# Performance work log

Hardware: AMD Instinct MI355X
Metric: run time of the kernel (lower is better)

The kernel has to match this reference:

```python
import jax, jax.numpy as jnp
from jax import lax
import numpy as np

B, T = 16, 64
NC, CS, HID, FEAT, ADIM = 32, 32, 128, 256, 6
CAT = NC * CS  # 1024


def _conv(x, w, b):
    # kernel 4, stride 2, padding 1 (NCHW / OIHW)
    y = lax.conv_general_dilated(x, w, window_strides=(2, 2), padding=[(1, 1), (1, 1)],
                                 dimension_numbers=('NCHW', 'OIHW', 'NCHW'))
    return y + b[None, :, None, None]


def _ln(x, g, b, eps=1e-5):
    # nn.LayerNorm([C,H,W]) normalizes over the last 3 dims with full affine
    m = jnp.mean(x, axis=(1, 2, 3), keepdims=True)
    v = jnp.var(x, axis=(1, 2, 3), keepdims=True)
    return (x - m) * lax.rsqrt(v + eps) * g[None] + b[None]


def setup_inputs() -> dict:
    key = jax.random.key(0)
    ks = jax.random.split(key, 12)
    w = lambda k, s: jax.random.normal(k, s, jnp.float32) * 0.02
    d = {
        'states': jax.random.normal(ks[0], (B, T, 3, 64, 64), jnp.float32),
        'actions': jax.random.normal(ks[1], (B, T, ADIM), jnp.float32),
        'conv1_w': w(ks[2], (32, 3, 4, 4)), 'conv1_b': jnp.zeros((32,), jnp.float32),
        'ln1_g': jnp.ones((32, 32, 32), jnp.float32), 'ln1_b': jnp.zeros((32, 32, 32), jnp.float32),
        'conv2_w': w(ks[3], (64, 32, 4, 4)), 'conv2_b': jnp.zeros((64,), jnp.float32),
        'ln2_g': jnp.ones((64, 16, 16), jnp.float32), 'ln2_b': jnp.zeros((64, 16, 16), jnp.float32),
        'conv3_w': w(ks[4], (128, 64, 4, 4)), 'conv3_b': jnp.zeros((128,), jnp.float32),
        'ln3_g': jnp.ones((128, 8, 8), jnp.float32), 'ln3_b': jnp.zeros((128, 8, 8), jnp.float32),
        'conv4_w': w(ks[5], (256, 128, 4, 4)), 'conv4_b': jnp.zeros((256,), jnp.float32),
        'ln4_g': jnp.ones((256, 4, 4), jnp.float32), 'ln4_b': jnp.zeros((256, 4, 4), jnp.float32),
        'fc_w': w(ks[6], (FEAT, 256 * 4 * 4)), 'fc_b': jnp.zeros((FEAT,), jnp.float32),
        'gru_wih': w(ks[7], (3 * HID, CAT + ADIM)), 'gru_whh': w(ks[8], (3 * HID, HID)),
        'gru_bih': jnp.zeros((3 * HID,), jnp.float32), 'gru_bhh': jnp.zeros((3 * HID,), jnp.float32),
        'prior_w': w(ks[9], (CAT, HID)), 'prior_b': jnp.zeros((CAT,), jnp.float32),
        'post_w': w(ks[10], (CAT, HID + FEAT)), 'post_b': jnp.zeros((CAT,), jnp.float32),
    }
    return d


def reference(states, actions, conv1_w, conv1_b, ln1_g, ln1_b, conv2_w, conv2_b, ln2_g, ln2_b,
              conv3_w, conv3_b, ln3_g, ln3_b, conv4_w, conv4_b, ln4_g, ln4_b, fc_w, fc_b,
              gru_wih, gru_whh, gru_bih, gru_bhh, prior_w, prior_b, post_w, post_b):
    bt = B * T
    # Encoder has no recurrent dependency -> batch all frames at once.
    x = states.reshape(bt, 3, 64, 64)
    x = jax.nn.silu(_ln(_conv(x, conv1_w, conv1_b), ln1_g, ln1_b))
    x = jax.nn.silu(_ln(_conv(x, conv2_w, conv2_b), ln2_g, ln2_b))
    x = jax.nn.silu(_ln(_conv(x, conv3_w, conv3_b), ln3_g, ln3_b))
    x = jax.nn.silu(_ln(_conv(x, conv4_w, conv4_b), ln4_g, ln4_b))
    feats = x.reshape(bt, -1) @ fc_w.T + fc_b              # [B*T, FEAT]
    feats = feats.reshape(B, T, FEAT).transpose(1, 0, 2)    # [T, B, FEAT]
    acts = actions.transpose(1, 0, 2)                       # [T, B, A]

    def step(carry, inp):
        h, z = carry
        a, f = inp
        xg = jnp.concatenate([z, a], axis=-1)
        gi = xg @ gru_wih.T + gru_bih
        gh = h @ gru_whh.T + gru_bhh
        ir, iz, inn = jnp.split(gi, 3, axis=-1)
        hr, hz, hn = jnp.split(gh, 3, axis=-1)
        r = jax.nn.sigmoid(ir + hr)
        u = jax.nn.sigmoid(iz + hz)
        n = jnp.tanh(inn + r * hn)
        h_new = (1.0 - u) * n + u * h                      # PyTorch GRUCell update
        prior = (h_new @ prior_w.T + prior_b).reshape(B, NC, CS)
        post = (jnp.concatenate([h_new, f], axis=-1) @ post_w.T + post_b).reshape(B, NC, CS)
        # eval-mode sampling: one-hot argmax (deterministic)
        z_new = jax.nn.one_hot(jnp.argmax(post, axis=-1), CS, dtype=h_new.dtype).reshape(B, CAT)
        return (h_new, z_new), (prior, post, h_new, z_new)

    init = (jnp.zeros((B, HID), states.dtype), jnp.zeros((B, CAT), states.dtype))
    _, (prior_l, post_l, h_seq, z_seq) = lax.scan(step, init, (acts, feats))
    return (prior_l.transpose(1, 0, 2, 3), post_l.transpose(1, 0, 2, 3),
            h_seq.transpose(1, 0, 2), z_seq.transpose(1, 0, 2))
```

## Files before the change

### kernel.cpp

```cpp
#include <hip/hip_runtime.h>
#include <math.h>


__device__ __forceinline__ float silu_f(float t){ return t / (1.f + __expf(-t)); }
__device__ __forceinline__ float sigm_f(float x){ return 1.f / (1.f + expf(-x)); }

__device__ __forceinline__ void block_stats_256(float s, float s2, int m,
                                                float& mean, float& rstd)
{
    __shared__ float red[8];
#pragma unroll
    for (int off = 32; off > 0; off >>= 1) {
        s  += __shfl_down(s, off);
        s2 += __shfl_down(s2, off);
    }
    int wv = threadIdx.x >> 6;
    if ((threadIdx.x & 63) == 0) { red[wv] = s; red[4 + wv] = s2; }
    __syncthreads();
    if (threadIdx.x == 0) {
        float S  = (red[0] + red[1]) + (red[2] + red[3]);
        float S2 = (red[4] + red[5]) + (red[6] + red[7]);
        float mu = S / m;
        float var = S2 / m - mu * mu;
        red[0] = mu;
        red[1] = rsqrtf(var + 1e-5f);
    }
    __syncthreads();
    mean = red[0]; rstd = red[1];
}

__global__ __launch_bounds__(256) void ln_fuse_k(float* __restrict__ x,
    const float* __restrict__ g, const float* __restrict__ b, int m)
{
    int n = blockIdx.x;
    float* p = x + (size_t)n * m;
    float s = 0.f, s2 = 0.f;
    for (int i = threadIdx.x * 4; i < m; i += 1024) {
        float4 v = *(const float4*)(p + i);
        s  += (v.x + v.y) + (v.z + v.w);
        s2 += (v.x*v.x + v.y*v.y) + (v.z*v.z + v.w*v.w);
    }
    float mean, rstd;
    block_stats_256(s, s2, m, mean, rstd);
    for (int i = threadIdx.x * 4; i < m; i += 1024) {
        float4 v  = *(float4*)(p + i);
        float4 gv = *(const float4*)(g + i);
        float4 bv = *(const float4*)(b + i);
        v.x = silu_f((v.x - mean) * rstd * gv.x + bv.x);
        v.y = silu_f((v.y - mean) * rstd * gv.y + bv.y);
        v.z = silu_f((v.z - mean) * rstd * gv.z + bv.z);
        v.w = silu_f((v.w - mean) * rstd * gv.w + bv.w);
        *(float4*)(p + i) = v;
    }
}

__global__ __launch_bounds__(256) void conv1_k(const float* __restrict__ in,
    const float* __restrict__ w, const float* __restrict__ bias, float* __restrict__ out)
{
    int n  = blockIdx.x;
    int yq = blockIdx.y;
    int tx = threadIdx.x & 31;
    int ty = threadIdx.x >> 5;
    int y  = yq * 8 + ty;
    const float* ip = in + (size_t)n * 12288;

    float okf[16]; int offs[16];
#pragma unroll
    for (int ky = 0; ky < 4; ky++) {
        int yy = 2 * y - 1 + ky;
        bool yok = ((unsigned)yy < 64u);
#pragma unroll
        for (int kx = 0; kx < 4; kx++) {
            int xx = 2 * tx - 1 + kx;
            bool ok = yok && ((unsigned)xx < 64u);
            okf[ky*4+kx]  = ok ? 1.f : 0.f;
            offs[ky*4+kx] = ok ? yy * 64 + xx : 0;
        }
    }
    float iv[48];
#pragma unroll
    for (int c = 0; c < 3; c++)
#pragma unroll
        for (int q = 0; q < 16; q++)
            iv[c*16+q] = ip[c*4096 + offs[q]] * okf[q];

    float* op = out + (size_t)n * 32768 + y * 32 + tx;
#pragma unroll 4
    for (int oc = 0; oc < 32; oc++) {
        float acc = bias[oc];
        const float* wp = w + oc * 48;
#pragma unroll
        for (int q = 0; q < 48; q++) acc += iv[q] * wp[q];
        op[oc * 1024] = acc;
    }
}

__global__ __launch_bounds__(256) void conv2_r(const float* __restrict__ in,
    const float* __restrict__ w, const float* __restrict__ bias, float* __restrict__ out)
{
    __shared__ __align__(16) float lds[8208];
    int n  = blockIdx.x;
    int tid = threadIdx.x;
    int wv  = tid >> 6;
    int g   = wv >> 1;
    int s   = ((wv & 1) << 6) | (tid & 63);
    int x   = s & 15, y0 = s >> 4;
    const float* ip = in + (size_t)n * 32768;

    int offs[2][16];
#pragma unroll
    for (int p = 0; p < 2; p++) {
        int y = y0 + 8 * p;
#pragma unroll
        for (int ky = 0; ky < 4; ky++) {
            int yi = 2 * y - 1 + ky;
#pragma unroll
            for (int kx = 0; kx < 4; kx++) {
                int xi = 2 * x - 1 + kx;
                bool ok = ((unsigned)yi < 32u) && ((unsigned)xi < 32u);
                int rot = ((xi >> 2) + (yi & 7)) & 7;
                int foff = yi * 32 + rot * 4 + (xi & 3);
                offs[p][ky*4+kx] = ok ? (4 + foff) * 4 : 0;
            }
        }
    }
    if (tid < 16) lds[(tid >> 2) * 1028 + (tid & 3)] = 0.f;

    float acc0[32], acc1[32];
#pragma unroll
    for (int i = 0; i < 32; i++) { float bv = bias[g*32 + i]; acc0[i] = bv; acc1[i] = bv; }

#pragma unroll 1
    for (int ch = 0; ch < 8; ch++) {
        __syncthreads();
        {
            const float4* gs = (const float4*)(ip + (ch << 12));
#pragma unroll
            for (int k = 0; k < 4; k++) {
                int gid = tid + (k << 8);
                int cc = gid >> 8, r = (gid >> 3) & 31, s4 = gid & 7;
                int rs = (s4 + (r & 7)) & 7;
                *(float4*)&lds[cc*1028 + 4 + r*32 + rs*4] = gs[gid];
            }
            int oc = tid >> 2, i4 = tid & 3;
            const float* wg = w + (size_t)oc * 512 + (ch << 6) + i4 * 4;
#pragma unroll
            for (int cc = 0; cc < 4; cc++)
                *(float4*)&lds[4112 + cc*1024 + oc*16 + i4*4] =
                    *(const float4*)(wg + cc * 16);
        }
        __syncthreads();
#pragma unroll 1
        for (int cc = 0; cc < 4; cc++) {
            const char* cb = (const char*)lds + cc * 4112;
            float iv0[16], iv1[16];
#pragma unroll
            for (int q = 0; q < 16; q++) {
                iv0[q] = *(const float*)(cb + offs[0][q]);
                iv1[q] = *(const float*)(cb + offs[1][q]);
            }
            const float* wb = &lds[4112 + cc*1024 + g*512];
#pragma unroll
            for (int o = 0; o < 32; o++) {
                float wt[16];
                *(float4*)&wt[0]  = *(const float4*)(wb + o*16);
                *(float4*)&wt[4]  = *(const float4*)(wb + o*16 + 4);
                *(float4*)&wt[8]  = *(const float4*)(wb + o*16 + 8);
                *(float4*)&wt[12] = *(const float4*)(wb + o*16 + 12);
#pragma unroll
                for (int q = 0; q < 16; q++) {
                    acc0[o] = fmaf(iv0[q], wt[q], acc0[o]);
                    acc1[o] = fmaf(iv1[q], wt[q], acc1[o]);
                }
            }
        }
    }
    float* op = out + (size_t)n * 16384;
#pragma unroll
    for (int o = 0; o < 32; o++) {
        op[(g*32 + o) * 256 + y0*16 + x]       = acc0[o];
        op[(g*32 + o) * 256 + (y0+8)*16 + x]   = acc1[o];
    }
}

__global__ __launch_bounds__(256) void conv3_r(const float* __restrict__ in,
    const float* __restrict__ w, const float* __restrict__ bias, float* __restrict__ out)
{
    __shared__ __align__(16) float lds[9232];
    int n   = blockIdx.x;
    int tid = threadIdx.x;
    int g   = tid >> 5;
    int slot= tid & 31;
    int x   = slot & 7, y0 = slot >> 3;

    int offs[2][16];
#pragma unroll
    for (int p = 0; p < 2; p++) {
        int y = y0 + 4 * p;
#pragma unroll
        for (int ky = 0; ky < 4; ky++) {
            int yi = 2 * y - 1 + ky;
#pragma unroll
            for (int kx = 0; kx < 4; kx++) {
                int xi = 2 * x - 1 + kx;
                bool ok = ((unsigned)yi < 16u) && ((unsigned)xi < 16u);
                int rot = ((xi >> 2) + (yi & 3)) & 3;
                int foff = yi * 16 + rot * 4 + (xi & 3);
                offs[p][ky*4+kx] = ok ? (4 + foff) * 4 : 0;
            }
        }
    }
    if (tid < 16) lds[(tid >> 2) * 260 + (tid & 3)] = 0.f;

    float acc0[16], acc1[16];
#pragma unroll
    for (int i = 0; i < 16; i++) { float bv = bias[g*16 + i]; acc0[i] = bv; acc1[i] = bv; }

    const float* ip = in + (size_t)n * 16384;
#pragma unroll 1
    for (int ch = 0; ch < 16; ch++) {
        __syncthreads();
        {
            const float4* gs = (const float4*)(ip + (ch << 10));
            int cc = tid >> 6, r = (tid >> 2) & 15, s4 = tid & 3;
            int rs = (s4 + (r & 3)) & 3;
            *(float4*)&lds[cc*260 + 4 + r*16 + rs*4] = gs[tid];
            int oc = tid >> 1, h = tid & 1;
            const float* wg = w + (size_t)oc * 1024 + (ch << 6) + h * 8;
#pragma unroll
            for (int c2 = 0; c2 < 4; c2++) {
                *(float4*)&lds[1040 + c2*2048 + oc*16 + h*8]     = *(const float4*)(wg + c2*16);
                *(float4*)&lds[1040 + c2*2048 + oc*16 + h*8 + 4] = *(const float4*)(wg + c2*16 + 4);
            }
        }
        __syncthreads();
#pragma unroll 1
        for (int cc = 0; cc < 4; cc++) {
            const char* cb = (const char*)lds + cc * 1040;
            float iv0[16], iv1[16];
#pragma unroll
            for (int q = 0; q < 16; q++) {
                iv0[q] = *(const float*)(cb + offs[0][q]);
                iv1[q] = *(const float*)(cb + offs[1][q]);
            }
            const float* wb = &lds[1040 + cc*2048 + g*256];
#pragma unroll
            for (int o = 0; o < 16; o++) {
                float wt[16];
                *(float4*)&wt[0]  = *(const float4*)(wb + o*16);
                *(float4*)&wt[4]  = *(const float4*)(wb + o*16 + 4);
                *(float4*)&wt[8]  = *(const float4*)(wb + o*16 + 8);
                *(float4*)&wt[12] = *(const float4*)(wb + o*16 + 12);
#pragma unroll
                for (int q = 0; q < 16; q++) {
                    acc0[o] = fmaf(iv0[q], wt[q], acc0[o]);
                    acc1[o] = fmaf(iv1[q], wt[q], acc1[o]);
                }
            }
        }
    }
    float* op = out + (size_t)n * 8192;
#pragma unroll
    for (int o = 0; o < 16; o++) {
        op[(g*16 + o) * 64 + slot]      = acc0[o];
        op[(g*16 + o) * 64 + slot + 32] = acc1[o];
    }
}

__global__ __launch_bounds__(256) void conv4_f(const float* __restrict__ in,
    const float* __restrict__ w, const float* __restrict__ bias,
    const float* __restrict__ g, const float* __restrict__ bet, float* __restrict__ out)
{
    int n  = blockIdx.x;
    int oc = threadIdx.x;
    const float* ip = in + (size_t)n * 8192;
    const float* wr = w + (size_t)oc * 2048;

    float acc[16];
#pragma unroll
    for (int s = 0; s < 16; s++) acc[s] = bias[oc];

    for (int c = 0; c < 128; c++) {
        const float* ic = ip + c * 64;
        const float* wc = wr + c * 16;
        float wf[16];
#pragma unroll
        for (int q = 0; q < 16; q += 4) {
            float4 v = *(const float4*)(wc + q);
            wf[q] = v.x; wf[q+1] = v.y; wf[q+2] = v.z; wf[q+3] = v.w;
        }
#pragma unroll
        for (int y = 0; y < 4; y++)
#pragma unroll
        for (int x = 0; x < 4; x++) {
            float a = acc[y * 4 + x];
#pragma unroll
            for (int ky = 0; ky < 4; ky++) {
                int yy = 2 * y - 1 + ky;
                if (yy < 0 || yy > 7) continue;
#pragma unroll
                for (int kx = 0; kx < 4; kx++) {
                    int xx = 2 * x - 1 + kx;
                    if (xx < 0 || xx > 7) continue;
                    a += wf[ky * 4 + kx] * ic[yy * 8 + xx];
                }
            }
            acc[y * 4 + x] = a;
        }
    }
    float s = 0.f, s2 = 0.f;
#pragma unroll
    for (int q = 0; q < 16; q++) { s += acc[q]; s2 += acc[q] * acc[q]; }
    float mean, rstd;
    block_stats_256(s, s2, 4096, mean, rstd);

    float* op = out + (size_t)n * 4096;
#pragma unroll
    for (int q = 0; q < 16; q++) {
        int flat = oc * 16 + q;
        float v = (acc[q] - mean) * rstd * g[flat] + bet[flat];
        op[flat] = silu_f(v);
    }
}

__global__ __launch_bounds__(256) void trfc_k(const float* __restrict__ w,
                                              float* __restrict__ wt)
{
    __shared__ float t[32][33];
    int bk = blockIdx.x * 32;
    int bj = blockIdx.y * 32;
    int lx = threadIdx.x & 31, ly = threadIdx.x >> 5;
#pragma unroll
    for (int s = 0; s < 4; s++)
        t[ly + 8*s][lx] = w[(size_t)(bj + ly + 8*s) * 4096 + bk + lx];
    __syncthreads();
#pragma unroll
    for (int s = 0; s < 4; s++)
        wt[(size_t)(bk + ly + 8*s) * 256 + bj + lx] = t[lx][ly + 8*s];
}

__global__ __launch_bounds__(256) void fc_k2(const float* __restrict__ a,
    const float* __restrict__ wT, const float* __restrict__ bias, float* __restrict__ o)
{
    int n0 = blockIdx.x * 8;
    int j  = threadIdx.x;
    float acc[8];
#pragma unroll
    for (int r = 0; r < 8; r++) acc[r] = 0.f;
    for (int k = 0; k < 4096; k += 4) {
        float wv0 = wT[(size_t)k * 256 + j];
        float wv1 = wT[(size_t)(k+1) * 256 + j];
        float wv2 = wT[(size_t)(k+2) * 256 + j];
        float wv3 = wT[(size_t)(k+3) * 256 + j];
#pragma unroll
        for (int r = 0; r < 8; r++) {
            const float* ar = a + (size_t)(n0 + r) * 4096 + k;
            acc[r] += wv0*ar[0] + wv1*ar[1] + wv2*ar[2] + wv3*ar[3];
        }
    }
    float bj = bias[j];
#pragma unroll
    for (int r = 0; r < 8; r++) o[(size_t)(n0 + r) * 256 + j] = acc[r] + bj;
}

__global__ __launch_bounds__(256) void fpost_k(const float* __restrict__ f,
    const float* __restrict__ w, const float* __restrict__ bias, float* __restrict__ o)
{
    int n0 = blockIdx.x * 4;
    int tid = threadIdx.x;
    float acc[4][4];
#pragma unroll
    for (int r = 0; r < 4; r++)
#pragma unroll
        for (int jj = 0; jj < 4; jj++) acc[r][jj] = 0.f;
    for (int k = 0; k < 256; k += 4) {
        float4 wv[4];
#pragma unroll
        for (int jj = 0; jj < 4; jj++)
            wv[jj] = *(const float4*)(w + (size_t)(tid + jj * 256) * 384 + 128 + k);
#pragma unroll
        for (int r = 0; r < 4; r++) {
            const float* fr = f + (size_t)(n0 + r) * 256 + k;
            float a0 = fr[0], a1 = fr[1], a2 = fr[2], a3 = fr[3];
#pragma unroll
            for (int jj = 0; jj < 4; jj++)
                acc[r][jj] += wv[jj].x*a0 + wv[jj].y*a1 + wv[jj].z*a2 + wv[jj].w*a3;
        }
    }
#pragma unroll
    for (int jj = 0; jj < 4; jj++) {
        float bj = bias[tid + jj * 256];
#pragma unroll
        for (int r = 0; r < 4; r++)
            o[(size_t)(n0 + r) * 1024 + tid + jj * 256] = acc[r][jj] + bj;
    }
}

__global__ __launch_bounds__(256) void prior_k(const float* __restrict__ h,
    const float* __restrict__ w, const float* __restrict__ bias, float* __restrict__ o)
{
    int n0 = blockIdx.x * 4;
    int tid = threadIdx.x;
    float acc[4][4];
#pragma unroll
    for (int r = 0; r < 4; r++)
#pragma unroll
        for (int jj = 0; jj < 4; jj++) acc[r][jj] = 0.f;
    for (int k = 0; k < 128; k += 4) {
        float4 wv[4];
#pragma unroll
        for (int jj = 0; jj < 4; jj++)
            wv[jj] = *(const float4*)(w + (size_t)(tid + jj * 256) * 128 + k);
#pragma unroll
        for (int r = 0; r < 4; r++) {
            const float* hr = h + (size_t)(n0 + r) * 128 + k;
            float a0 = hr[0], a1 = hr[1], a2 = hr[2], a3 = hr[3];
#pragma unroll
            for (int jj = 0; jj < 4; jj++)
                acc[r][jj] += wv[jj].x*a0 + wv[jj].y*a1 + wv[jj].z*a2 + wv[jj].w*a3;
        }
    }
#pragma unroll
    for (int jj = 0; jj < 4; jj++) {
        float bj = bias[tid + jj * 256];
#pragma unroll
        for (int r = 0; r < 4; r++)
            o[(size_t)(n0 + r) * 1024 + tid + jj * 256] = acc[r][jj] + bj;
    }
}

__global__ __launch_bounds__(128) void ai_k(const float* __restrict__ act,
    const float* __restrict__ wih, const float* __restrict__ bih, float* __restrict__ o)
{
    int n = blockIdx.x;
    int j = blockIdx.y * 128 + threadIdx.x;
    const float* ar = act + (size_t)n * 6;
    const float* wr = wih + (size_t)j * 1030 + 1024;
    float acc = bih[j];
#pragma unroll
    for (int k = 0; k < 6; k++) acc += ar[k] * wr[k];
    o[(size_t)n * 384 + j] = acc;
}

__global__ __launch_bounds__(256) void tr_k(const float* __restrict__ wih,
                                            float* __restrict__ wt)
{
    int g = blockIdx.x * 256 + threadIdx.x;
    int k = g / 384;
    int j = g - k * 384;
    wt[g] = wih[(size_t)j * 1030 + k];
}

__global__ __launch_bounds__(256) void tr_whh_k(const float* __restrict__ whh,
                                                float* __restrict__ wt)
{
    int g = blockIdx.x * 256 + threadIdx.x;
    int c  = g & 3;
    int jk = g >> 2;
    int j  = jk % 384;
    int k4 = jk / 384;
    wt[g] = whh[(size_t)j * 128 + k4 * 4 + c];
}

__global__ __launch_bounds__(256) void tr_pw_k(const float* __restrict__ pw,
                                               float* __restrict__ wt)
{
    int g = blockIdx.x * 256 + threadIdx.x;
    int c  = g & 3;
    int jk = g >> 2;
    int j  = jk & 1023;
    int k4 = jk >> 10;
    wt[g] = pw[(size_t)j * 384 + k4 * 4 + c];
}

__global__ __launch_bounds__(1024) void gru_k(const float* __restrict__ wihT,
    const float* __restrict__ whhV, const float* __restrict__ bhh,
    const float* __restrict__ ai, const float* __restrict__ fpost,
    const float* __restrict__ pwV, float* __restrict__ out)
{
    float* out_post = out + 1048576;
    float* out_h    = out + 2097152;
    float* out_z    = out + 2228224;
    int b   = blockIdx.x;
    int tid = threadIdx.x;
    __shared__ __align__(16) float h[128];
    __shared__ float gi[384], gh[384];
    __shared__ int idx[32];
    if (tid < 128) h[tid] = 0.f;
    __syncthreads();

    const float4* h4  = (const float4*)h;
    const float4* wv4 = (const float4*)whhV;
    const float4* pv4 = (const float4*)pwV;

    for (int t = 0; t < 64; t++) {
        int n = b * 64 + t;
        if (tid < 384) {
            float a = ai[(size_t)n * 384 + tid];
            if (t > 0) {
#pragma unroll 8
                for (int c = 0; c < 32; c++)
                    a += wihT[(size_t)(c * 32 + idx[c]) * 384 + tid];
            }
            gi[tid] = a;
            float a2 = bhh[tid];
#pragma unroll 8
            for (int k4 = 0; k4 < 32; k4++) {
                float4 wq = wv4[k4 * 384 + tid];
                float4 hq = h4[k4];
                a2 += wq.x*hq.x + wq.y*hq.y + wq.z*hq.z + wq.w*hq.w;
            }
            gh[tid] = a2;
        }
        __syncthreads();
        if (tid < 128) {
            float r  = sigm_f(gi[tid] + gh[tid]);
            float u  = sigm_f(gi[128 + tid] + gh[128 + tid]);
            float nn = tanhf(gi[256 + tid] + r * gh[256 + tid]);
            float hn = (1.f - u) * nn + u * h[tid];
            h[tid] = hn;
            out_h[(size_t)n * 128 + tid] = hn;
        }
        __syncthreads();
        if (tid < 512) {
            float a0 = fpost[(size_t)n * 1024 + tid];
            float a1 = fpost[(size_t)n * 1024 + 512 + tid];
#pragma unroll 8
            for (int k4 = 0; k4 < 32; k4++) {
                float4 hq = h4[k4];
                float4 w0 = pv4[k4 * 1024 + tid];
                float4 w1 = pv4[k4 * 1024 + 512 + tid];
                a0 += w0.x*hq.x + w0.y*hq.y + w0.z*hq.z + w0.w*hq.w;
                a1 += w1.x*hq.x + w1.y*hq.y + w1.z*hq.z + w1.w*hq.w;
            }
            out_post[(size_t)n * 1024 + tid]       = a0;
            out_post[(size_t)n * 1024 + 512 + tid] = a1;

            float b0 = a0, b1 = a1;
            int i0 = tid & 31, i1 = tid & 31;
#pragma unroll
            for (int m = 16; m >= 1; m >>= 1) {
                float ob0 = __shfl_xor(b0, m);
                int   oi0 = __shfl_xor(i0, m);
                float ob1 = __shfl_xor(b1, m);
                int   oi1 = __shfl_xor(i1, m);
                if (ob0 > b0 || (ob0 == b0 && oi0 < i0)) { b0 = ob0; i0 = oi0; }
                if (ob1 > b1 || (ob1 == b1 && oi1 < i1)) { b1 = ob1; i1 = oi1; }
            }
            out_z[(size_t)n * 1024 + tid]       = ((tid & 31) == i0) ? 1.f : 0.f;
            out_z[(size_t)n * 1024 + 512 + tid] = ((tid & 31) == i1) ? 1.f : 0.f;
            if ((tid & 31) == 0) {
                idx[tid >> 5]        = i0;
                idx[(tid >> 5) + 16] = i1;
            }
        }
        __syncthreads();
    }
}

extern "C" void kernel_launch(void* const* d_in, const int* in_sizes, int n_in,
                              void* d_out, int out_size, void* d_ws, size_t ws_size,
                              hipStream_t stream)
{
    const float* states  = (const float*)d_in[0];
    const float* actions = (const float*)d_in[1];
    const float* c1w = (const float*)d_in[2];  const float* c1b = (const float*)d_in[3];
    const float* l1g = (const float*)d_in[4];  const float* l1b = (const float*)d_in[5];
    const float* c2w = (const float*)d_in[6];  const float* c2b = (const float*)d_in[7];
    const float* l2g = (const float*)d_in[8];  const float* l2b = (const float*)d_in[9];
    const float* c3w = (const float*)d_in[10]; const float* c3b = (const float*)d_in[11];
    const float* l3g = (const float*)d_in[12]; const float* l3b = (const float*)d_in[13];
    const float* c4w = (const float*)d_in[14]; const float* c4b = (const float*)d_in[15];
    const float* l4g = (const float*)d_in[16]; const float* l4b = (const float*)d_in[17];
    const float* fcw = (const float*)d_in[18]; const float* fcb = (const float*)d_in[19];
    const float* wih = (const float*)d_in[20]; const float* whh = (const float*)d_in[21];
    const float* bih = (const float*)d_in[22]; const float* bhh = (const float*)d_in[23];
    const float* prw = (const float*)d_in[24]; const float* prb = (const float*)d_in[25];
    const float* pw  = (const float*)d_in[26]; const float* pb  = (const float*)d_in[27];

    float* out = (float*)d_out;
    float* ws  = (float*)d_ws;

    size_t S = 64;
    {
        const size_t cands[4] = {1024, 512, 256, 128};
        for (int i = 0; i < 4; i++) {
            size_t need = (cands[i] * 49152ull + 3325952ull) * 4ull;
            if (need <= ws_size) { S = cands[i]; break; }
        }
    }
    int C = (int)(1024 / S);

    float* bufA  = ws;
    float* bufB  = bufA + S * 32768;
    float* feats = bufB + S * 16384;
    float* fpost = feats + 262144;
    float* aibuf = fpost + 1048576;
    float* wihT  = aibuf + 393216;
    float* fcwT  = wihT + 393216;
    float* whhV  = fcwT + 1048576;
    float* pwV   = whhV + 49152;

    trfc_k<<<dim3(128, 8), 256, 0, stream>>>(fcw, fcwT);
    tr_whh_k<<<192, 256, 0, stream>>>(whh, whhV);
    tr_pw_k<<<512, 256, 0, stream>>>(pw, pwV);

    for (int cc = 0; cc < C; cc++) {
        size_t n0 = (size_t)cc * S;
        conv1_k<<<dim3((unsigned)S, 4), 256, 0, stream>>>(states + n0 * 12288, c1w, c1b, bufA);
        ln_fuse_k<<<(unsigned)S, 256, 0, stream>>>(bufA, l1g, l1b, 32768);
        conv2_r<<<(unsigned)S, 256, 0, stream>>>(bufA, c2w, c2b, bufB);
        ln_fuse_k<<<(unsigned)S, 256, 0, stream>>>(bufB, l2g, l2b, 16384);
        conv3_r<<<(unsigned)S, 256, 0, stream>>>(bufB, c3w, c3b, bufA);
        ln_fuse_k<<<(unsigned)S, 256, 0, stream>>>(bufA, l3g, l3b, 8192);
        conv4_f<<<(unsigned)S, 256, 0, stream>>>(bufA, c4w, c4b, l4g, l4b, bufB);
        fc_k2<<<(unsigned)(S / 8), 256, 0, stream>>>(bufB, fcwT, fcb, feats + n0 * 256);
    }

    fpost_k<<<256, 256, 0, stream>>>(feats, pw, pb, fpost);
    ai_k<<<dim3(1024, 3), 128, 0, stream>>>(actions, wih, bih, aibuf);
    tr_k<<<1536, 256, 0, stream>>>(wih, wihT);

    gru_k<<<16, 1024, 0, stream>>>(wihT, whhV, bhh, aibuf, fpost, pwV, out);
    prior_k<<<256, 256, 0, stream>>>(out + 2097152, prw, prb, out);
}
```

Baseline: 2.512 ms.

## Split GRU recurrence across producer/consumer blocks with global-memory flag sync

Measured after the change: 2.951 ms. 1.18x slower.

```diff
diff --git a/kernel.cpp b/kernel.cpp
--- a/kernel.cpp
+++ b/kernel.cpp
@@ -473,28 +473,51 @@
     wt[g] = pw[(size_t)j * 384 + k4 * 4 + c];
 }
 
-__global__ __launch_bounds__(1024) void gru_k(const float* __restrict__ wihT,
-    const float* __restrict__ whhV, const float* __restrict__ bhh,
-    const float* __restrict__ ai, const float* __restrict__ fpost,
-    const float* __restrict__ pwV, float* __restrict__ out)
-{
-    float* out_post = out + 1048576;
-    float* out_h    = out + 2097152;
-    float* out_z    = out + 2228224;
+__global__ __launch_bounds__(256) void sync0_k(int* __restrict__ flags)
+{
+    if (threadIdx.x < 144) flags[threadIdx.x] = 0;
+}
+
+
+__device__ __forceinline__ void gru_g_role(float* smem,
+    const float* __restrict__ wihT, const float* __restrict__ whhV,
+    const float* __restrict__ bhh, const float* __restrict__ ai,
+    float* hbuf, int* idxbuf, int* hflag, int* pflag, float* out)
+{
+    float* h  = smem;
+    float* gi = smem + 128;
+    float* gh = smem + 512;
+    int*   idx = (int*)(smem + 896);
     int b   = blockIdx.x;
     int tid = threadIdx.x;
-    __shared__ __align__(16) float h[128];
-    __shared__ float gi[384], gh[384];
-    __shared__ int idx[32];
+
+    const float4* wv4 = (const float4*)whhV;
+    float4 wq[32];
+    if (tid < 384) {
+#pragma unroll
+        for (int k4 = 0; k4 < 32; k4++) wq[k4] = wv4[k4 * 384 + tid];
+    }
     if (tid < 128) h[tid] = 0.f;
     __syncthreads();
 
-    const float4* h4  = (const float4*)h;
-    const float4* wv4 = (const float4*)whhV;
-    const float4* pv4 = (const float4*)pwV;
-
+    float* out_h = out + 2097152;
     for (int t = 0; t < 64; t++) {
         int n = b * 64 + t;
+        if (t > 0) {
+            if (tid < 8) {
+                int guard = 0;
+                while (__hip_atomic_load(&pflag[b*8 + tid], __ATOMIC_ACQUIRE,
+                                         __HIP_MEMORY_SCOPE_AGENT) < t) {
+                    __builtin_amdgcn_s_sleep(1);
+                    if (++guard > (1 << 25)) break;
+                }
+            }
+            __syncthreads();
+            if (tid < 32)
+                idx[tid] = __hip_atomic_load(&idxbuf[b*32 + tid], __ATOMIC_RELAXED,
+                                             __HIP_MEMORY_SCOPE_AGENT);
+            __syncthreads();
+        }
         if (tid < 384) {
             float a = ai[(size_t)n * 384 + tid];
             if (t > 0) {
@@ -504,11 +527,12 @@
             }
             gi[tid] = a;
             float a2 = bhh[tid];
-#pragma unroll 8
+            const float4* h4 = (const float4*)h;
+#pragma unroll
             for (int k4 = 0; k4 < 32; k4++) {
-                float4 wq = wv4[k4 * 384 + tid];
                 float4 hq = h4[k4];
-                a2 += wq.x*hq.x + wq.y*hq.y + wq.z*hq.z + wq.w*hq.w;
+                float4 w  = wq[k4];
+                a2 += w.x*hq.x + w.y*hq.y + w.z*hq.z + w.w*hq.w;
             }
             gh[tid] = a2;
         }
@@ -520,42 +544,102 @@
             float hn = (1.f - u) * nn + u * h[tid];
             h[tid] = hn;
             out_h[(size_t)n * 128 + tid] = hn;
-        }
-        __syncthreads();
-        if (tid < 512) {
-            float a0 = fpost[(size_t)n * 1024 + tid];
-            float a1 = fpost[(size_t)n * 1024 + 512 + tid];
-#pragma unroll 8
-            for (int k4 = 0; k4 < 32; k4++) {
+            __hip_atomic_store(&hbuf[b*128 + tid], hn, __ATOMIC_RELAXED,
+                               __HIP_MEMORY_SCOPE_AGENT);
+        }
+        __syncthreads();
+        if (tid == 0)
+            __hip_atomic_store(&hflag[b], t + 1, __ATOMIC_RELEASE,
+                               __HIP_MEMORY_SCOPE_AGENT);
+    }
+}
+
+__device__ __forceinline__ void gru_p_role(float* smem,
+    const float* __restrict__ pwV, const float* __restrict__ fpost,
+    float* hbuf, int* idxbuf, int* hflag, int* pflag, float* out)
+{
+    float* wlds = smem;
+    float* hl   = smem + 15872;
+    int bp  = blockIdx.x - 16;
+    int b   = bp >> 3, p = bp & 7;
+    int tid = threadIdx.x;
+
+    const float4* pv4 = (const float4*)pwV;
+    float4* wl4 = (float4*)wlds;
+    float4 w31 = make_float4(0.f, 0.f, 0.f, 0.f);
+    if (tid < 128) {
+        int j = p * 128 + tid;
+#pragma unroll 1
+        for (int k4 = 0; k4 < 31; k4++) wl4[k4 * 128 + tid] = pv4[k4 * 1024 + j];
+        w31 = pv4[31 * 1024 + j];
+    }
+    __syncthreads();
+
+    float* out_post = out + 1048576;
+    float* out_z    = out + 2228224;
+    for (int t = 0; t < 64; t++) {
+        int n = b * 64 + t;
+        int j = p * 128 + (tid & 127);
+        float fp = 0.f;
+        if (tid < 128) fp = fpost[(size_t)n * 1024 + j];
+        if (tid == 0) {
+            int guard = 0;
+            while (__hip_atomic_load(&hflag[b], __ATOMIC_ACQUIRE,
+                                     __HIP_MEMORY_SCOPE_AGENT) < t + 1) {
+                __builtin_amdgcn_s_sleep(1);
+                if (++guard > (1 << 25)) break;
+            }
+        }
+        __syncthreads();
+        if (tid < 128)
+            hl[tid] = __hip_atomic_load(&hbuf[b*128 + tid], __ATOMIC_RELAXED,
+                                        __HIP_MEMORY_SCOPE_AGENT);
+        __syncthreads();
+        if (tid < 128) {
+            const float4* h4 = (const float4*)hl;
+            float acc = fp;
+#pragma unroll
+            for (int k4 = 0; k4 < 31; k4++) {
+                float4 w  = wl4[k4 * 128 + tid];
                 float4 hq = h4[k4];
-                float4 w0 = pv4[k4 * 1024 + tid];
-                float4 w1 = pv4[k4 * 1024 + 512 + tid];
-                a0 += w0.x*hq.x + w0.y*hq.y + w0.z*hq.z + w0.w*hq.w;
-                a1 += w1.x*hq.x + w1.y*hq.y + w1.z*hq.z + w1.w*hq.w;
-            }
-            out_post[(size_t)n * 1024 + tid]       = a0;
-            out_post[(size_t)n * 1024 + 512 + tid] = a1;
-
-            float b0 = a0, b1 = a1;
-            int i0 = tid & 31, i1 = tid & 31;
+                acc += w.x*hq.x + w.y*hq.y + w.z*hq.z + w.w*hq.w;
+            }
+            {
+                float4 hq = h4[31];
+                acc += w31.x*hq.x + w31.y*hq.y + w31.z*hq.z + w31.w*hq.w;
+            }
+            out_post[(size_t)n * 1024 + j] = acc;
+
+            float bb = acc; int ii = tid & 31;
 #pragma unroll
             for (int m = 16; m >= 1; m >>= 1) {
-                float ob0 = __shfl_xor(b0, m);
-                int   oi0 = __shfl_xor(i0, m);
-                float ob1 = __shfl_xor(b1, m);
-                int   oi1 = __shfl_xor(i1, m);
-                if (ob0 > b0 || (ob0 == b0 && oi0 < i0)) { b0 = ob0; i0 = oi0; }
-                if (ob1 > b1 || (ob1 == b1 && oi1 < i1)) { b1 = ob1; i1 = oi1; }
-            }
-            out_z[(size_t)n * 1024 + tid]       = ((tid & 31) == i0) ? 1.f : 0.f;
-            out_z[(size_t)n * 1024 + 512 + tid] = ((tid & 31) == i1) ? 1.f : 0.f;
-            if ((tid & 31) == 0) {
-                idx[tid >> 5]        = i0;
-                idx[(tid >> 5) + 16] = i1;
-            }
-        }
-        __syncthreads();
-    }
+                float ob = __shfl_xor(bb, m);
+                int   oi = __shfl_xor(ii, m);
+                if (ob > bb || (ob == bb && oi < ii)) { bb = ob; ii = oi; }
+            }
+            out_z[(size_t)n * 1024 + j] = ((tid & 31) == ii) ? 1.f : 0.f;
+            if ((tid & 31) == 0)
+                __hip_atomic_store(&idxbuf[b*32 + p*4 + (tid >> 5)], ii,
+                                   __ATOMIC_RELAXED, __HIP_MEMORY_SCOPE_AGENT);
+        }
+        __syncthreads();
+        if (tid == 0)
+            __hip_atomic_store(&pflag[b*8 + p], t + 1, __ATOMIC_RELEASE,
+                               __HIP_MEMORY_SCOPE_AGENT);
+    }
+}
+
+__global__ __launch_bounds__(512) void gru_sync(
+    const float* __restrict__ wihT, const float* __restrict__ whhV,
+    const float* __restrict__ bhh, const float* __restrict__ ai,
+    const float* __restrict__ fpost, const float* __restrict__ pwV,
+    float* hbuf, int* idxbuf, int* hflag, int* pflag, float* out)
+{
+    __shared__ __align__(16) float smem[16000];
+    if (blockIdx.x < 16)
+        gru_g_role(smem, wihT, whhV, bhh, ai, hbuf, idxbuf, hflag, pflag, out);
+    else
+        gru_p_role(smem, pwV, fpost, hbuf, idxbuf, hflag, pflag, out);
 }
 
 extern "C" void kernel_launch(void* const* d_in, const int* in_sizes, int n_in,
@@ -585,7 +669,7 @@
     {
         const size_t cands[4] = {1024, 512, 256, 128};
         for (int i = 0; i < 4; i++) {
-            size_t need = (cands[i] * 49152ull + 3325952ull) * 4ull;
+            size_t need = (cands[i] * 49152ull + 3330048ull) * 4ull;
             if (need <= ws_size) { S = cands[i]; break; }
         }
     }
@@ -600,7 +684,12 @@
     float* fcwT  = wihT + 393216;
     float* whhV  = fcwT + 1048576;
     float* pwV   = whhV + 49152;
-
+    float* hbuf  = pwV + 131072;
+    int*   idxbuf = (int*)(hbuf + 2048);
+    int*   hflag  = idxbuf + 512;
+    int*   pflag  = hflag + 16;
+
+    sync0_k<<<1, 256, 0, stream>>>(hflag);
     trfc_k<<<dim3(128, 8), 256, 0, stream>>>(fcw, fcwT);
     tr_whh_k<<<192, 256, 0, stream>>>(whh, whhV);
     tr_pw_k<<<512, 256, 0, stream>>>(pw, pwV);
@@ -621,6 +710,7 @@
     ai_k<<<dim3(1024, 3), 128, 0, stream>>>(actions, wih, bih, aibuf);
     tr_k<<<1536, 256, 0, stream>>>(wih, wihT);
 
-    gru_k<<<16, 1024, 0, stream>>>(wihT, whhV, bhh, aibuf, fpost, pwV, out);
+    gru_sync<<<144, 512, 0, stream>>>(wihT, whhV, bhh, aibuf, fpost, pwV,
+                                      hbuf, idxbuf, hflag, pflag, out);
     prior_k<<<256, 256, 0, stream>>>(out + 2097152, prw, prb, out);
 }
```

## Keep GRU and posterior weights in registers and merge recurrent matvec into post pass

Applied to the files above, without the earlier changes.

Result: slower. 3.546 ms (+41.2%).

```diff
diff --git a/kernel.cpp b/kernel.cpp
--- a/kernel.cpp
+++ b/kernel.cpp
@@ -486,12 +486,33 @@
     __shared__ __align__(16) float h[128];
     __shared__ float gi[384], gh[384];
     __shared__ int idx[32];
-    if (tid < 128) h[tid] = 0.f;
-    __syncthreads();
-
-    const float4* h4  = (const float4*)h;
+
     const float4* wv4 = (const float4*)whhV;
     const float4* pv4 = (const float4*)pwV;
+
+    float4 pwr[32];
+#pragma unroll
+    for (int k4 = 0; k4 < 32; k4++) {
+        pwr[k4] = pv4[k4 * 1024 + tid];
+        asm volatile("" : "+v"(pwr[k4].x), "+v"(pwr[k4].y),
+                          "+v"(pwr[k4].z), "+v"(pwr[k4].w));
+    }
+    float4 whr[32];
+    float bhh_r = 0.f;
+    if (tid < 384) {
+        bhh_r = bhh[tid];
+#pragma unroll
+        for (int k4 = 0; k4 < 32; k4++) {
+            whr[k4] = wv4[k4 * 384 + tid];
+            asm volatile("" : "+v"(whr[k4].x), "+v"(whr[k4].y),
+                              "+v"(whr[k4].z), "+v"(whr[k4].w));
+        }
+    }
+    if (tid < 128) h[tid] = 0.f;
+    if (tid < 384) gh[tid] = bhh_r;
+    __syncthreads();
+
+    const float4* h4 = (const float4*)h;
 
     for (int t = 0; t < 64; t++) {
         int n = b * 64 + t;
@@ -503,14 +524,6 @@
                     a += wihT[(size_t)(c * 32 + idx[c]) * 384 + tid];
             }
             gi[tid] = a;
-            float a2 = bhh[tid];
-#pragma unroll 8
-            for (int k4 = 0; k4 < 32; k4++) {
-                float4 wq = wv4[k4 * 384 + tid];
-                float4 hq = h4[k4];
-                a2 += wq.x*hq.x + wq.y*hq.y + wq.z*hq.z + wq.w*hq.w;
-            }
-            gh[tid] = a2;
         }
         __syncthreads();
         if (tid < 128) {
@@ -522,38 +535,34 @@
             out_h[(size_t)n * 128 + tid] = hn;
         }
         __syncthreads();
-        if (tid < 512) {
-            float a0 = fpost[(size_t)n * 1024 + tid];
-            float a1 = fpost[(size_t)n * 1024 + 512 + tid];
-#pragma unroll 8
+        float a0 = fpost[(size_t)n * 1024 + tid];
+        if (tid < 384) {
+            float a2 = bhh_r;
+#pragma unroll
             for (int k4 = 0; k4 < 32; k4++) {
                 float4 hq = h4[k4];
-                float4 w0 = pv4[k4 * 1024 + tid];
-                float4 w1 = pv4[k4 * 1024 + 512 + tid];
-                a0 += w0.x*hq.x + w0.y*hq.y + w0.z*hq.z + w0.w*hq.w;
-                a1 += w1.x*hq.x + w1.y*hq.y + w1.z*hq.z + w1.w*hq.w;
-            }
-            out_post[(size_t)n * 1024 + tid]       = a0;
-            out_post[(size_t)n * 1024 + 512 + tid] = a1;
-
-            float b0 = a0, b1 = a1;
-            int i0 = tid & 31, i1 = tid & 31;
-#pragma unroll
-            for (int m = 16; m >= 1; m >>= 1) {
-                float ob0 = __shfl_xor(b0, m);
-                int   oi0 = __shfl_xor(i0, m);
-                float ob1 = __shfl_xor(b1, m);
-                int   oi1 = __shfl_xor(i1, m);
-                if (ob0 > b0 || (ob0 == b0 && oi0 < i0)) { b0 = ob0; i0 = oi0; }
-                if (ob1 > b1 || (ob1 == b1 && oi1 < i1)) { b1 = ob1; i1 = oi1; }
-            }
-            out_z[(size_t)n * 1024 + tid]       = ((tid & 31) == i0) ? 1.f : 0.f;
-            out_z[(size_t)n * 1024 + 512 + tid] = ((tid & 31) == i1) ? 1.f : 0.f;
-            if ((tid & 31) == 0) {
-                idx[tid >> 5]        = i0;
-                idx[(tid >> 5) + 16] = i1;
-            }
-        }
+                a0 += pwr[k4].x*hq.x + pwr[k4].y*hq.y + pwr[k4].z*hq.z + pwr[k4].w*hq.w;
+                a2 += whr[k4].x*hq.x + whr[k4].y*hq.y + whr[k4].z*hq.z + whr[k4].w*hq.w;
+            }
+            gh[tid] = a2;
+        } else {
+#pragma unroll
+            for (int k4 = 0; k4 < 32; k4++) {
+                float4 hq = h4[k4];
+                a0 += pwr[k4].x*hq.x + pwr[k4].y*hq.y + pwr[k4].z*hq.z + pwr[k4].w*hq.w;
+            }
+        }
+        out_post[(size_t)n * 1024 + tid] = a0;
+
+        float b0 = a0; int i0 = tid & 31;
+#pragma unroll
+        for (int m = 16; m >= 1; m >>= 1) {
+            float ob = __shfl_xor(b0, m);
+            int   oi = __shfl_xor(i0, m);
+            if (ob > b0 || (ob == b0 && oi < i0)) { b0 = ob; i0 = oi; }
+        }
+        out_z[(size_t)n * 1024 + tid] = ((tid & 31) == i0) ? 1.f : 0.f;
+        if ((tid & 31) == 0) idx[tid >> 5] = i0;
         __syncthreads();
     }
 }
```

## Cache post weights in registers and fold hidden matvec into post phase

Applied to the files above, without the earlier changes.

Measured after the change: 3.567 ms. 1.42x slower.

```diff
diff --git a/kernel.cpp b/kernel.cpp
--- a/kernel.cpp
+++ b/kernel.cpp
@@ -473,7 +473,7 @@
     wt[g] = pw[(size_t)j * 384 + k4 * 4 + c];
 }
 
-__global__ __launch_bounds__(1024) void gru_k(const float* __restrict__ wihT,
+__global__ __launch_bounds__(512) void gru_k(const float* __restrict__ wihT,
     const float* __restrict__ whhV, const float* __restrict__ bhh,
     const float* __restrict__ ai, const float* __restrict__ fpost,
     const float* __restrict__ pwV, float* __restrict__ out)
@@ -486,15 +486,28 @@
     __shared__ __align__(16) float h[128];
     __shared__ float gi[384], gh[384];
     __shared__ int idx[32];
-    if (tid < 128) h[tid] = 0.f;
-    __syncthreads();
-
-    const float4* h4  = (const float4*)h;
+
     const float4* wv4 = (const float4*)whhV;
     const float4* pv4 = (const float4*)pwV;
 
+    float4 pwr[32];
+#pragma unroll
+    for (int k4 = 0; k4 < 32; k4++) {
+        pwr[k4] = pv4[k4 * 1024 + tid];
+        asm volatile("" : "+v"(pwr[k4].x), "+v"(pwr[k4].y),
+                          "+v"(pwr[k4].z), "+v"(pwr[k4].w));
+    }
+    float bhh_r = (tid < 384) ? bhh[tid] : 0.f;
+    if (tid < 128) h[tid] = 0.f;
+    if (tid < 384) gh[tid] = bhh_r;
+    __syncthreads();
+
+    const float4* h4 = (const float4*)h;
+
     for (int t = 0; t < 64; t++) {
         int n = b * 64 + t;
+        float f0 = fpost[(size_t)n * 1024 + tid];
+        float f1 = fpost[(size_t)n * 1024 + 512 + tid];
         if (tid < 384) {
             float a = ai[(size_t)n * 384 + tid];
             if (t > 0) {
@@ -503,14 +516,6 @@
                     a += wihT[(size_t)(c * 32 + idx[c]) * 384 + tid];
             }
             gi[tid] = a;
-            float a2 = bhh[tid];
-#pragma unroll 8
-            for (int k4 = 0; k4 < 32; k4++) {
-                float4 wq = wv4[k4 * 384 + tid];
-                float4 hq = h4[k4];
-                a2 += wq.x*hq.x + wq.y*hq.y + wq.z*hq.z + wq.w*hq.w;
-            }
-            gh[tid] = a2;
         }
         __syncthreads();
         if (tid < 128) {
@@ -522,37 +527,47 @@
             out_h[(size_t)n * 128 + tid] = hn;
         }
         __syncthreads();
-        if (tid < 512) {
-            float a0 = fpost[(size_t)n * 1024 + tid];
-            float a1 = fpost[(size_t)n * 1024 + 512 + tid];
-#pragma unroll 8
+        float a0 = f0, a1 = f1;
+        if (tid < 384) {
+            float a2 = bhh_r;
+#pragma unroll
             for (int k4 = 0; k4 < 32; k4++) {
                 float4 hq = h4[k4];
-                float4 w0 = pv4[k4 * 1024 + tid];
                 float4 w1 = pv4[k4 * 1024 + 512 + tid];
-                a0 += w0.x*hq.x + w0.y*hq.y + w0.z*hq.z + w0.w*hq.w;
+                float4 w2 = wv4[k4 * 384 + tid];
+                a0 += pwr[k4].x*hq.x + pwr[k4].y*hq.y + pwr[k4].z*hq.z + pwr[k4].w*hq.w;
                 a1 += w1.x*hq.x + w1.y*hq.y + w1.z*hq.z + w1.w*hq.w;
-            }
-            out_post[(size_t)n * 1024 + tid]       = a0;
-            out_post[(size_t)n * 1024 + 512 + tid] = a1;
-
-            float b0 = a0, b1 = a1;
-            int i0 = tid & 31, i1 = tid & 31;
-#pragma unroll
-            for (int m = 16; m >= 1; m >>= 1) {
-                float ob0 = __shfl_xor(b0, m);
-                int   oi0 = __shfl_xor(i0, m);
-                float ob1 = __shfl_xor(b1, m);
-                int   oi1 = __shfl_xor(i1, m);
-                if (ob0 > b0 || (ob0 == b0 && oi0 < i0)) { b0 = ob0; i0 = oi0; }
-                if (ob1 > b1 || (ob1 == b1 && oi1 < i1)) { b1 = ob1; i1 = oi1; }
-            }
-            out_z[(size_t)n * 1024 + tid]       = ((tid & 31) == i0) ? 1.f : 0.f;
-            out_z[(size_t)n * 1024 + 512 + tid] = ((tid & 31) == i1) ? 1.f : 0.f;
-            if ((tid & 31) == 0) {
-                idx[tid >> 5]        = i0;
-                idx[(tid >> 5) + 16] = i1;
-            }
+                a2 += w2.x*hq.x + w2.y*hq.y + w2.z*hq.z + w2.w*hq.w;
+            }
+            gh[tid] = a2;
+        } else {
+#pragma unroll
+            for (int k4 = 0; k4 < 32; k4++) {
+                float4 hq = h4[k4];
+                float4 w1 = pv4[k4 * 1024 + 512 + tid];
+                a0 += pwr[k4].x*hq.x + pwr[k4].y*hq.y + pwr[k4].z*hq.z + pwr[k4].w*hq.w;
+                a1 += w1.x*hq.x + w1.y*hq.y + w1.z*hq.z + w1.w*hq.w;
+            }
+        }
+        out_post[(size_t)n * 1024 + tid]       = a0;
+        out_post[(size_t)n * 1024 + 512 + tid] = a1;
+
+        float b0 = a0, b1 = a1;
+        int i0 = tid & 31, i1 = tid & 31;
+#pragma unroll
+        for (int m = 16; m >= 1; m >>= 1) {
+            float ob0 = __shfl_xor(b0, m);
+            int   oi0 = __shfl_xor(i0, m);
+            float ob1 = __shfl_xor(b1, m);
+            int   oi1 = __shfl_xor(i1, m);
+            if (ob0 > b0 || (ob0 == b0 && oi0 < i0)) { b0 = ob0; i0 = oi0; }
+            if (ob1 > b1 || (ob1 == b1 && oi1 < i1)) { b1 = ob1; i1 = oi1; }
+        }
+        out_z[(size_t)n * 1024 + tid]       = ((tid & 31) == i0) ? 1.f : 0.f;
+        out_z[(size_t)n * 1024 + 512 + tid] = ((tid & 31) == i1) ? 1.f : 0.f;
+        if ((tid & 31) == 0) {
+            idx[tid >> 5]        = i0;
+            idx[(tid >> 5) + 16] = i1;
         }
         __syncthreads();
     }
@@ -621,6 +636,6 @@
     ai_k<<<dim3(1024, 3), 128, 0, stream>>>(actions, wih, bih, aibuf);
     tr_k<<<1536, 256, 0, stream>>>(wih, wihT);
 
-    gru_k<<<16, 1024, 0, stream>>>(wihT, whhV, bhh, aibuf, fpost, pwV, out);
+    gru_k<<<16, 512, 0, stream>>>(wihT, whhV, bhh, aibuf, fpost, pwV, out);
     prior_k<<<256, 256, 0, stream>>>(out + 2097152, prw, prb, out);
 }
```
